# Kernel tuning notes

Hardware: AMD Instinct MI355X
Metric: run time of the kernel (lower is better)

## Reference

```python
import jax, jax.numpy as jnp
import numpy as np

HIDDEN_DIM = 768
N_HEAD = 12
ATTN_DIM = HIDDEN_DIM // N_HEAD  # 64
SCALE = jnp.sqrt(jnp.float32(ATTN_DIM))


def setup_inputs() -> dict:
    key = jax.random.key(0)
    ks = jax.random.split(key, 6)
    B, S = 8, 2048
    return {
        "query": jax.random.normal(ks[0], (B, S, HIDDEN_DIM), dtype=jnp.float32),
        "key": jax.random.normal(ks[1], (B, S, HIDDEN_DIM), dtype=jnp.float32),
        "value": jax.random.normal(ks[2], (B, S, HIDDEN_DIM), dtype=jnp.float32),
        "Wq": jax.random.normal(ks[3], (ATTN_DIM, HIDDEN_DIM), dtype=jnp.float32) * 0.02,
        "Wk": jax.random.normal(ks[4], (ATTN_DIM, HIDDEN_DIM), dtype=jnp.float32) * 0.02,
        "Wv": jax.random.normal(ks[5], (ATTN_DIM, HIDDEN_DIM), dtype=jnp.float32) * 0.02,
    }


def reference(query, key, value, Wq, Wk, Wv):
    # Linear projections (bias=False): x @ W.T -> [B, S, attn_dim]
    q = jnp.einsum("bsh,dh->bsd", query, Wq)
    k = jnp.einsum("bsh,dh->bsd", key, Wk)
    v = jnp.einsum("bsh,dh->bsd", value, Wv)
    # Scaled dot-product scores: [B, S, S]
    scores = jnp.einsum("bqd,bkd->bqk", q, k) / SCALE
    attn = jax.nn.softmax(scores, axis=-1)  # dropout p=0 -> identity in eval
    # Weighted sum of values: [B, S, attn_dim]
    return jnp.einsum("bqk,bkd->bqd", attn, v)
```

## Files before the change

### kernel.cpp

```cpp
#include <hip/hip_runtime.h>

typedef short s16x8 __attribute__((ext_vector_type(8)));
typedef float f32x4 __attribute__((ext_vector_type(4)));
typedef unsigned short us4 __attribute__((ext_vector_type(4)));

static __device__ __forceinline__ unsigned short f2bf(float f) {
  unsigned u = __builtin_bit_cast(unsigned, f);
  u += 0x7FFFu + ((u >> 16) & 1u);
  return (unsigned short)(u >> 16);
}

#define MFMA16(a, b, c) __builtin_amdgcn_mfma_f32_16x16x32_bf16((a), (b), (c), 0, 0, 0)

__global__ __launch_bounds__(256) void proj_kernel(
    const float* __restrict__ Xq, const float* __restrict__ Xk, const float* __restrict__ Xv,
    const float* __restrict__ Wq, const float* __restrict__ Wk, const float* __restrict__ Wv,
    unsigned short* __restrict__ q_out,
    unsigned short* __restrict__ kf_out,
    unsigned short* __restrict__ vf_out)
{
  __shared__ __align__(16) unsigned short xs[64][72];
  __shared__ __align__(16) unsigned short ws[64][72];

  const int bid = blockIdx.x;
  const int t = bid >> 8;
  const int rb = bid & 255;
  const int b = rb >> 5;
  const int stile = rb & 31;
  const float* X = (t == 0) ? Xq : (t == 1) ? Xk : Xv;
  const float* W = (t == 0) ? Wq : (t == 1) ? Wk : Wv;

  const int tid = threadIdx.x;
  const int wv = tid >> 6;
  const int lane = tid & 63;
  const int j = lane & 15;
  const int g = lane >> 4;

  f32x4 acc[4];
#pragma unroll
  for (int i = 0; i < 4; ++i) acc[i] = {0.f, 0.f, 0.f, 0.f};

  const size_t xrow0 = (size_t)b * 2048 + (size_t)stile * 64;

  for (int kc = 0; kc < 768; kc += 64) {
#pragma unroll
    for (int p = 0; p < 4; ++p) {
      int lin = p * 256 + tid;
      int row = lin >> 4;
      int seg = lin & 15;
      float4 xv = *(const float4*)(X + (xrow0 + row) * 768 + kc + seg * 4);
      us4 px; px.x = f2bf(xv.x); px.y = f2bf(xv.y); px.z = f2bf(xv.z); px.w = f2bf(xv.w);
      *(us4*)&xs[row][seg * 4] = px;
      float4 wv4 = *(const float4*)(W + (size_t)row * 768 + kc + seg * 4);
      us4 pw; pw.x = f2bf(wv4.x); pw.y = f2bf(wv4.y); pw.z = f2bf(wv4.z); pw.w = f2bf(wv4.w);
      *(us4*)&ws[row][seg * 4] = pw;
    }
    __syncthreads();
    s16x8 a0 = *(const s16x8*)&xs[wv * 16 + j][g * 8];
    s16x8 a1 = *(const s16x8*)&xs[wv * 16 + j][32 + g * 8];
#pragma unroll
    for (int ct = 0; ct < 4; ++ct) {
      s16x8 b0 = *(const s16x8*)&ws[ct * 16 + j][g * 8];
      s16x8 b1 = *(const s16x8*)&ws[ct * 16 + j][32 + g * 8];
      acc[ct] = MFMA16(a0, b0, acc[ct]);
      acc[ct] = MFMA16(a1, b1, acc[ct]);
    }
    __syncthreads();
  }

  if (t == 0) {
    unsigned short* out = q_out + (xrow0 + (size_t)wv * 16) * 64;
#pragma unroll
    for (int ct = 0; ct < 4; ++ct)
#pragma unroll
      for (int r = 0; r < 4; ++r)
        out[(g * 4 + r) * 64 + ct * 16 + j] = f2bf(acc[ct][r] * 0.125f);
  } else {
    unsigned short* fb = &xs[0][0];
    if (t == 1) {
#pragma unroll
      for (int ct = 0; ct < 4; ++ct) {
        int base16 = wv * 1024 + ((ct >= 2) ? 512 : 0) + (((ct & 1) * 2 + (j >> 3)) * 128) + (j & 7);
#pragma unroll
        for (int r = 0; r < 4; ++r)
          fb[base16 + (g * 4 + r) * 8] = f2bf(acc[ct][r]);
      }
    } else {
#pragma unroll
      for (int ct = 0; ct < 4; ++ct) {
        us4 pk;
        pk.x = f2bf(acc[ct][0]); pk.y = f2bf(acc[ct][1]);
        pk.z = f2bf(acc[ct][2]); pk.w = f2bf(acc[ct][3]);
        *(us4*)&fb[ct * 1024 + ((wv >= 2) ? 512 : 0) +
                   (((wv & 1) * 2 + (g >> 1)) * 16 + j) * 8 + (g & 1) * 4] = pk;
      }
    }
    __syncthreads();
    unsigned short* gb = (t == 1) ? kf_out + ((size_t)b * 128 + stile * 4) * 1024
                                  : vf_out + ((size_t)b * 32 + stile) * 4096;
#pragma unroll
    for (int p2 = 0; p2 < 2; ++p2) {
      int idx = p2 * 2048 + tid * 8;
      *(s16x8*)(gb + idx) = *(const s16x8*)&fb[idx];
    }
  }
}

__global__ __launch_bounds__(256, 4) void attn_kernel(
    const unsigned short* __restrict__ qg,
    const unsigned short* __restrict__ kf,
    const unsigned short* __restrict__ vf,
    float* __restrict__ out)
{
  __shared__ __align__(16) unsigned short p_lds[4][16][72];
  __shared__ __align__(16) float comb[4][16][68];
  __shared__ float mls[4][16];
  __shared__ float lls[4][16];

  const int tid = threadIdx.x;
  const int wv = tid >> 6;
  const int lane = tid & 63;
  const int j = lane & 15;
  const int g = lane >> 4;

  const int bid0 = blockIdx.x;
  const int bid = (bid0 & 7) * 128 + (bid0 >> 3);
  const int b = bid >> 7;
  const int qtile = bid & 127;
  const int qbase = qtile * 16;

  const unsigned short* qp = qg + (((size_t)b * 2048) + qbase) * 64;
  s16x8 q0 = *(const s16x8*)(qp + j * 64 + g * 8);
  s16x8 q1 = *(const s16x8*)(qp + j * 64 + 32 + g * 8);

  f32x4 o[4];
#pragma unroll
  for (int i = 0; i < 4; ++i) o[i] = {0.f, 0.f, 0.f, 0.f};
  float m = -1e30f, l = 0.f;

  const int kv0 = wv * 512;
  const unsigned short* kfb = kf + ((size_t)b * 128 + (kv0 >> 4)) * 1024 + lane * 8;
  const unsigned short* vfb = vf + ((size_t)b * 32 + (kv0 >> 6)) * 4096 + lane * 8;

  for (int kt = 0; kt < 8; ++kt) {
    const unsigned short* kc_ = kfb + kt * 4096;
    s16x8 ka[4], kb2[4];
#pragma unroll
    for (int ct = 0; ct < 4; ++ct) {
      ka[ct] = *(const s16x8*)(kc_ + ct * 1024);
      kb2[ct] = *(const s16x8*)(kc_ + ct * 1024 + 512);
    }
    f32x4 st[4];
#pragma unroll
    for (int ct = 0; ct < 4; ++ct) {
      f32x4 z = {0.f, 0.f, 0.f, 0.f};
      z = MFMA16(ka[ct], q0, z);
      z = MFMA16(kb2[ct], q1, z);
      st[ct] = z;
    }
    const unsigned short* vc_ = vfb + kt * 4096;
    s16x8 va[4], vb2[4];
#pragma unroll
    for (int dt = 0; dt < 4; ++dt) {
      va[dt] = *(const s16x8*)(vc_ + dt * 1024);
      vb2[dt] = *(const s16x8*)(vc_ + dt * 1024 + 512);
    }
    float cmax = -1e30f;
#pragma unroll
    for (int ct = 0; ct < 4; ++ct)
#pragma unroll
      for (int r = 0; r < 4; ++r) cmax = fmaxf(cmax, st[ct][r]);
    cmax = fmaxf(cmax, __shfl_xor(cmax, 16));
    cmax = fmaxf(cmax, __shfl_xor(cmax, 32));
    if (!__all(cmax <= m + 6.0f)) {
      const float mnew = fmaxf(m, cmax);
      const float alpha = __expf(m - mnew);
      m = mnew;
      l *= alpha;
#pragma unroll
      for (int r = 0; r < 4; ++r) {
        float a_r = __shfl(alpha, g * 4 + r);
#pragma unroll
        for (int dt = 0; dt < 4; ++dt) o[dt][r] *= a_r;
      }
    }
    float rs = 0.f;
#pragma unroll
    for (int ct = 0; ct < 4; ++ct) {
      float p0 = __expf(st[ct][0] - m);
      float p1 = __expf(st[ct][1] - m);
      float p2 = __expf(st[ct][2] - m);
      float p3 = __expf(st[ct][3] - m);
      rs += (p0 + p1) + (p2 + p3);
      us4 pk; pk.x = f2bf(p0); pk.y = f2bf(p1); pk.z = f2bf(p2); pk.w = f2bf(p3);
      *(us4*)&p_lds[wv][j][ct * 16 + g * 4] = pk;
    }
    rs += __shfl_xor(rs, 16);
    rs += __shfl_xor(rs, 32);
    l += rs;
    s16x8 pa0 = *(const s16x8*)&p_lds[wv][j][g * 8];
    s16x8 pa1 = *(const s16x8*)&p_lds[wv][j][32 + g * 8];
#pragma unroll
    for (int dt = 0; dt < 4; ++dt) {
      o[dt] = MFMA16(pa0, va[dt], o[dt]);
      o[dt] = MFMA16(pa1, vb2[dt], o[dt]);
    }
  }

#pragma unroll
  for (int dt = 0; dt < 4; ++dt)
#pragma unroll
    for (int r = 0; r < 4; ++r)
      comb[wv][g * 4 + r][dt * 16 + j] = o[dt][r];
  if (g == 0) { mls[wv][j] = m; lls[wv][j] = l; }
  __syncthreads();

#pragma unroll
  for (int rr = 0; rr < 4; ++rr) {
    const int row = wv * 4 + rr;
    float m0 = mls[0][row], m1 = mls[1][row], m2 = mls[2][row], m3 = mls[3][row];
    float M = fmaxf(fmaxf(m0, m1), fmaxf(m2, m3));
    float w0 = __expf(m0 - M), w1 = __expf(m1 - M);
    float w2 = __expf(m2 - M), w3 = __expf(m3 - M);
    float acc = comb[0][row][lane] * w0 + comb[1][row][lane] * w1 +
                comb[2][row][lane] * w2 + comb[3][row][lane] * w3;
    float lt = lls[0][row] * w0 + lls[1][row] * w1 +
               lls[2][row] * w2 + lls[3][row] * w3;
    out[(((size_t)b * 2048) + qbase + row) * 64 + lane] = acc / lt;
  }
}

extern "C" void kernel_launch(void* const* d_in, const int* in_sizes, int n_in,
                              void* d_out, int out_size, void* d_ws, size_t ws_size,
                              hipStream_t stream) {
  const float* query = (const float*)d_in[0];
  const float* key_  = (const float*)d_in[1];
  const float* value = (const float*)d_in[2];
  const float* Wq = (const float*)d_in[3];
  const float* Wk = (const float*)d_in[4];
  const float* Wv = (const float*)d_in[5];

  unsigned short* qb = (unsigned short*)d_ws;
  unsigned short* kfb = qb + 1048576u;
  unsigned short* vfb = qb + 2u * 1048576u;
  float* outp = (float*)d_out;

  hipLaunchKernelGGL(proj_kernel, dim3(768), dim3(256), 0, stream,
                     query, key_, value, Wq, Wk, Wv, qb, kfb, vfb);
  hipLaunchKernelGGL(attn_kernel, dim3(1024), dim3(256), 0, stream,
                     qb, kfb, vfb, outp);
}
```

Baseline: 52.80 us.

## Pre-convert weights to bf16 fragments and drop LDS staging in projection

Adds a small kernel that converts and pre-scales Wq/Wk/Wv into bf16 MFMA fragment layout once per call. The projection kernel now has each wave own a 16-row chunk and load X straight from global into registers with double-buffered prefetch, removing LDS staging and the per-iteration block barriers. Q is also stored in fragment layout so the attention kernel reads it with contiguous vector loads. This costs an extra kernel launch and more registers per thread, and weight fragments are re-read from global by every wave.

```diff
diff --git a/kernel.cpp b/kernel.cpp
--- a/kernel.cpp
+++ b/kernel.cpp
@@ -10,104 +10,128 @@
   return (unsigned short)(u >> 16);
 }
 
+static __device__ __forceinline__ s16x8 pack8(float4 a, float4 b) {
+  s16x8 r;
+  r[0] = (short)f2bf(a.x); r[1] = (short)f2bf(a.y);
+  r[2] = (short)f2bf(a.z); r[3] = (short)f2bf(a.w);
+  r[4] = (short)f2bf(b.x); r[5] = (short)f2bf(b.y);
+  r[6] = (short)f2bf(b.z); r[7] = (short)f2bf(b.w);
+  return r;
+}
+
+static __device__ __forceinline__ s16x8 pack8s(float4 a, float4 b, float sc) {
+  s16x8 r;
+  r[0] = (short)f2bf(a.x * sc); r[1] = (short)f2bf(a.y * sc);
+  r[2] = (short)f2bf(a.z * sc); r[3] = (short)f2bf(a.w * sc);
+  r[4] = (short)f2bf(b.x * sc); r[5] = (short)f2bf(b.y * sc);
+  r[6] = (short)f2bf(b.z * sc); r[7] = (short)f2bf(b.w * sc);
+  return r;
+}
+
 #define MFMA16(a, b, c) __builtin_amdgcn_mfma_f32_16x16x32_bf16((a), (b), (c), 0, 0, 0)
 
-__global__ __launch_bounds__(256) void proj_kernel(
-    const float* __restrict__ Xq, const float* __restrict__ Xk, const float* __restrict__ Xv,
-    const float* __restrict__ Wq, const float* __restrict__ Wk, const float* __restrict__ Wv,
-    unsigned short* __restrict__ q_out,
-    unsigned short* __restrict__ kf_out,
-    unsigned short* __restrict__ vf_out)
+__global__ __launch_bounds__(256) void wconv_kernel(
+    const float* __restrict__ Wq, const float* __restrict__ Wk,
+    const float* __restrict__ Wv, unsigned short* __restrict__ wf) {
+  const int t = blockIdx.x / 24, g24 = blockIdx.x % 24;
+  const int wv = threadIdx.x >> 6, lane = threadIdx.x & 63;
+  const int j = lane & 15, g = lane >> 4;
+  const int grp = g24 * 4 + wv;
+  const int kc = grp >> 3, r3 = grp & 7, ct = r3 >> 1, h = r3 & 1;
+  const float* W = (t == 0) ? Wq : (t == 1) ? Wk : Wv;
+  const float* p = W + (size_t)(ct * 16 + j) * 768 + kc * 64 + h * 32 + g * 8;
+  float4 w0 = *(const float4*)p;
+  float4 w1 = *(const float4*)(p + 4);
+  const float sc = (t == 0) ? 0.125f : 1.0f;
+  *(s16x8*)(wf + (size_t)t * 49152 + grp * 512 + lane * 8) = pack8s(w0, w1, sc);
+}
+
+__global__ __launch_bounds__(256, 3) void proj_kernel(
+    const float* __restrict__ Xq, const float* __restrict__ Xk,
+    const float* __restrict__ Xv, const unsigned short* __restrict__ wf,
+    unsigned short* __restrict__ qf,
+    unsigned short* __restrict__ kf,
+    unsigned short* __restrict__ vfo)
 {
-  __shared__ __align__(16) unsigned short xs[64][72];
-  __shared__ __align__(16) unsigned short ws[64][72];
-
-  const int bid = blockIdx.x;
-  const int t = bid >> 8;
-  const int rb = bid & 255;
-  const int b = rb >> 5;
-  const int stile = rb & 31;
-  const float* X = (t == 0) ? Xq : (t == 1) ? Xk : Xv;
-  const float* W = (t == 0) ? Wq : (t == 1) ? Wk : Wv;
-
+  __shared__ __align__(16) unsigned short fb[4][4096];
   const int tid = threadIdx.x;
   const int wv = tid >> 6;
   const int lane = tid & 63;
   const int j = lane & 15;
   const int g = lane >> 4;
 
+  const int gid = blockIdx.x * 4 + wv;
+  const int t = gid >> 10;
+  const int chunk = gid & 1023;
+  const float* X = (t == 0) ? Xq : (t == 1) ? Xk : Xv;
+  const float* xb = X + (size_t)(chunk * 16 + j) * 768 + g * 8;
+  const unsigned short* wfb = wf + (size_t)t * 49152 + lane * 8;
+
   f32x4 acc[4];
 #pragma unroll
   for (int i = 0; i < 4; ++i) acc[i] = {0.f, 0.f, 0.f, 0.f};
 
-  const size_t xrow0 = (size_t)b * 2048 + (size_t)stile * 64;
-
-  for (int kc = 0; kc < 768; kc += 64) {
-#pragma unroll
-    for (int p = 0; p < 4; ++p) {
-      int lin = p * 256 + tid;
-      int row = lin >> 4;
-      int seg = lin & 15;
-      float4 xv = *(const float4*)(X + (xrow0 + row) * 768 + kc + seg * 4);
-      us4 px; px.x = f2bf(xv.x); px.y = f2bf(xv.y); px.z = f2bf(xv.z); px.w = f2bf(xv.w);
-      *(us4*)&xs[row][seg * 4] = px;
-      float4 wv4 = *(const float4*)(W + (size_t)row * 768 + kc + seg * 4);
-      us4 pw; pw.x = f2bf(wv4.x); pw.y = f2bf(wv4.y); pw.z = f2bf(wv4.z); pw.w = f2bf(wv4.w);
-      *(us4*)&ws[row][seg * 4] = pw;
-    }
-    __syncthreads();
-    s16x8 a0 = *(const s16x8*)&xs[wv * 16 + j][g * 8];
-    s16x8 a1 = *(const s16x8*)&xs[wv * 16 + j][32 + g * 8];
-#pragma unroll
-    for (int ct = 0; ct < 4; ++ct) {
-      s16x8 b0 = *(const s16x8*)&ws[ct * 16 + j][g * 8];
-      s16x8 b1 = *(const s16x8*)&ws[ct * 16 + j][32 + g * 8];
-      acc[ct] = MFMA16(a0, b0, acc[ct]);
-      acc[ct] = MFMA16(a1, b1, acc[ct]);
-    }
-    __syncthreads();
-  }
-
-  if (t == 0) {
-    unsigned short* out = q_out + (xrow0 + (size_t)wv * 16) * 64;
-#pragma unroll
-    for (int ct = 0; ct < 4; ++ct)
-#pragma unroll
-      for (int r = 0; r < 4; ++r)
-        out[(g * 4 + r) * 64 + ct * 16 + j] = f2bf(acc[ct][r] * 0.125f);
+  float4 xr[2][4];
+  s16x8 br[2][8];
+  {
+    const float* p = xb;
+    xr[0][0] = *(const float4*)p;        xr[0][1] = *(const float4*)(p + 4);
+    xr[0][2] = *(const float4*)(p + 32); xr[0][3] = *(const float4*)(p + 36);
+    const unsigned short* q = wfb;
+#pragma unroll
+    for (int i = 0; i < 8; ++i) br[0][i] = *(const s16x8*)(q + i * 512);
+  }
+#pragma unroll
+  for (int kk = 0; kk < 12; ++kk) {
+    const int cur = kk & 1, nxt = cur ^ 1;
+    if (kk < 11) {
+      const float* p = xb + (kk + 1) * 64;
+      xr[nxt][0] = *(const float4*)p;        xr[nxt][1] = *(const float4*)(p + 4);
+      xr[nxt][2] = *(const float4*)(p + 32); xr[nxt][3] = *(const float4*)(p + 36);
+      const unsigned short* q = wfb + (size_t)(kk + 1) * 4096;
+#pragma unroll
+      for (int i = 0; i < 8; ++i) br[nxt][i] = *(const s16x8*)(q + i * 512);
+    }
+    s16x8 a0 = pack8(xr[cur][0], xr[cur][1]);
+    s16x8 a1 = pack8(xr[cur][2], xr[cur][3]);
+#pragma unroll
+    for (int ct = 0; ct < 4; ++ct) {
+      acc[ct] = MFMA16(a0, br[cur][ct * 2], acc[ct]);
+      acc[ct] = MFMA16(a1, br[cur][ct * 2 + 1], acc[ct]);
+    }
+  }
+
+  unsigned short* myfb = fb[wv];
+  if (t < 2) {
+#pragma unroll
+    for (int ct = 0; ct < 4; ++ct) {
+      const int base = (ct >> 1) * 512 + (((ct & 1) * 2 + (j >> 3)) * 128) + (j & 7);
+#pragma unroll
+      for (int r = 0; r < 4; ++r) myfb[base + (g * 4 + r) * 8] = f2bf(acc[ct][r]);
+    }
+    unsigned short* dst = ((t == 0) ? qf : kf) + (size_t)chunk * 1024;
+    *(s16x8*)(dst + lane * 8) = *(const s16x8*)(myfb + lane * 8);
+    *(s16x8*)(dst + 512 + lane * 8) = *(const s16x8*)(myfb + 512 + lane * 8);
   } else {
-    unsigned short* fb = &xs[0][0];
-    if (t == 1) {
-#pragma unroll
-      for (int ct = 0; ct < 4; ++ct) {
-        int base16 = wv * 1024 + ((ct >= 2) ? 512 : 0) + (((ct & 1) * 2 + (j >> 3)) * 128) + (j & 7);
-#pragma unroll
-        for (int r = 0; r < 4; ++r)
-          fb[base16 + (g * 4 + r) * 8] = f2bf(acc[ct][r]);
+    const int q4 = chunk & 3;
+#pragma unroll
+    for (int ct = 0; ct < 4; ++ct) {
+#pragma unroll
+      for (int r = 0; r < 4; ++r) {
+        const int sl = q4 * 16 + g * 4 + r;
+        myfb[ct * 1024 + (sl >> 5) * 512 + (((sl & 31) >> 3) * 16 + j) * 8 + (sl & 7)] =
+            f2bf(acc[ct][r]);
       }
-    } else {
-#pragma unroll
-      for (int ct = 0; ct < 4; ++ct) {
-        us4 pk;
-        pk.x = f2bf(acc[ct][0]); pk.y = f2bf(acc[ct][1]);
-        pk.z = f2bf(acc[ct][2]); pk.w = f2bf(acc[ct][3]);
-        *(us4*)&fb[ct * 1024 + ((wv >= 2) ? 512 : 0) +
-                   (((wv & 1) * 2 + (g >> 1)) * 16 + j) * 8 + (g & 1) * 4] = pk;
-      }
-    }
-    __syncthreads();
-    unsigned short* gb = (t == 1) ? kf_out + ((size_t)b * 128 + stile * 4) * 1024
-                                  : vf_out + ((size_t)b * 32 + stile) * 4096;
-#pragma unroll
-    for (int p2 = 0; p2 < 2; ++p2) {
-      int idx = p2 * 2048 + tid * 8;
-      *(s16x8*)(gb + idx) = *(const s16x8*)&fb[idx];
-    }
+    }
+    unsigned short* dst = vfo + (size_t)(chunk >> 2) * 4096 + q4 * 256 + lane * 4;
+#pragma unroll
+    for (int s = 0; s < 4; ++s)
+      *(us4*)(dst + s * 1024) = *(const us4*)(myfb + s * 1024 + q4 * 256 + lane * 4);
   }
 }
 
 __global__ __launch_bounds__(256, 4) void attn_kernel(
-    const unsigned short* __restrict__ qg,
+    const unsigned short* __restrict__ qf,
     const unsigned short* __restrict__ kf,
     const unsigned short* __restrict__ vf,
     float* __restrict__ out)
@@ -129,9 +153,9 @@
   const int qtile = bid & 127;
   const int qbase = qtile * 16;
 
-  const unsigned short* qp = qg + (((size_t)b * 2048) + qbase) * 64;
-  s16x8 q0 = *(const s16x8*)(qp + j * 64 + g * 8);
-  s16x8 q1 = *(const s16x8*)(qp + j * 64 + 32 + g * 8);
+  const unsigned short* qfb = qf + ((size_t)(b * 128 + qtile)) * 1024 + lane * 8;
+  s16x8 q0 = *(const s16x8*)(qfb);
+  s16x8 q1 = *(const s16x8*)(qfb + 512);
 
   f32x4 o[4];
 #pragma unroll
@@ -240,13 +264,16 @@
   const float* Wk = (const float*)d_in[4];
   const float* Wv = (const float*)d_in[5];
 
-  unsigned short* qb = (unsigned short*)d_ws;
-  unsigned short* kfb = qb + 1048576u;
-  unsigned short* vfb = qb + 2u * 1048576u;
+  unsigned short* qfb = (unsigned short*)d_ws;
+  unsigned short* kfb = qfb + 1048576u;
+  unsigned short* vfb = qfb + 2u * 1048576u;
+  unsigned short* wfb = qfb + 3u * 1048576u;
   float* outp = (float*)d_out;
 
+  hipLaunchKernelGGL(wconv_kernel, dim3(72), dim3(256), 0, stream,
+                     Wq, Wk, Wv, wfb);
   hipLaunchKernelGGL(proj_kernel, dim3(768), dim3(256), 0, stream,
-                     query, key_, value, Wq, Wk, Wv, qb, kfb, vfb);
+                     query, key_, value, wfb, qfb, kfb, vfb);
   hipLaunchKernelGGL(attn_kernel, dim3(1024), dim3(256), 0, stream,
-                     qb, kfb, vfb, outp);
-}
+                     qfb, kfb, vfb, outp);
+}
```

Result: slower. 56.95 us (+7.9%).
